# Performance work log

Measured on AMD Instinct MI355X. Metric: run time of the kernel, lower is better.

The kernel has to match this reference:

```python
import jax, jax.numpy as jnp
import numpy as np

N = 100000      # nodes
E = 1600000     # edges
F_IN = 128      # num_node_features
C = 8           # num_classes
EPS = 1e-5


def _lin_init(key, fi, fo):
    k1, k2 = jax.random.split(key)
    s = 1.0 / np.sqrt(fi)
    W = jax.random.uniform(k1, (fi, fo), jnp.float32, -s, s)
    b = jax.random.uniform(k2, (fo,), jnp.float32, -s, s)
    return W, b


def _bn_init(key, f):
    k1, k2, k3, k4 = jax.random.split(key, 4)
    gamma = 1.0 + 0.1 * jax.random.normal(k1, (f,), jnp.float32)
    beta = 0.1 * jax.random.normal(k2, (f,), jnp.float32)
    mean = 0.1 * jax.random.normal(k3, (f,), jnp.float32)
    var = jax.random.uniform(k4, (f,), jnp.float32, 0.5, 1.5)
    return gamma, beta, mean, var


def setup_inputs() -> dict:
    key = jax.random.key(0)
    ks = jax.random.split(key, 10)
    p = {}
    p["x"] = jax.random.normal(ks[0], (N, F_IN), jnp.float32)
    p["edge_index"] = jax.random.randint(ks[1], (2, E), 0, N, jnp.int32)
    p["W1"], p["b1"] = _lin_init(ks[2], F_IN, 64)
    p["g1"], p["be1"], p["m1"], p["v1"] = _bn_init(ks[3], 64)
    p["W2"], p["b2"] = _lin_init(ks[4], 64, 32)
    p["g2"], p["be2"], p["m2"], p["v2"] = _bn_init(ks[5], 32)
    p["W3"], p["b3"] = _lin_init(ks[6], 32, 16)
    p["g3"], p["be3"], p["m3"], p["v3"] = _bn_init(ks[7], 16)
    p["fcW"], p["fcb"] = _lin_init(ks[8], 16, C)
    return p


def _gcn_conv(h, W, b, src, dst, dinv):
    # GCNConv: transform, then symmetric-normalized aggregation with self-loops.
    hw = h @ W                                   # [N, Fout]
    coef = (dinv[src] * dinv[dst])[:, None]      # [E, 1]
    agg = jax.ops.segment_sum(hw[src] * coef, dst, num_segments=N)
    agg = agg + hw * (dinv * dinv)[:, None]      # self-loop contribution
    return agg + b


def _bn(h, g, be, m, v):
    # eval-mode BatchNorm1d with running stats
    return g * (h - m) * jax.lax.rsqrt(v + EPS) + be


def reference(x, edge_index, W1, b1, g1, be1, m1, v1, W2, b2, g2, be2, m2, v2,
              W3, b3, g3, be3, m3, v3, fcW, fcb):
    src, dst = edge_index[0], edge_index[1]
    deg = jax.ops.segment_sum(jnp.ones((E,), jnp.float32), dst, num_segments=N) + 1.0
    dinv = jax.lax.rsqrt(deg)                    # deg >= 1 due to self-loops

    h = jax.nn.relu(_bn(_gcn_conv(x, W1, b1, src, dst, dinv), g1, be1, m1, v1))
    h = jax.nn.relu(_bn(_gcn_conv(h, W2, b2, src, dst, dinv), g2, be2, m2, v2))
    h = jax.nn.relu(_bn(_gcn_conv(h, W3, b3, src, dst, dinv), g3, be3, m3, v3))
    return jax.nn.sigmoid(h @ fcW + fcb)
```

## Files before the change

### kernel.cpp

```cpp
#include <hip/hip_runtime.h>
#include <math.h>

static constexpr int NN = 100000;
static constexpr int NE = 1600000;
static constexpr float BN_EPS = 1e-5f;
static constexpr int K_BKT = (NN + 255) / 256;
static constexpr int CH = 4096;

typedef __attribute__((ext_vector_type(8))) short bf16x8;
typedef __attribute__((ext_vector_type(4))) float f32x4;

__device__ __forceinline__ unsigned short f2bf(float f) {
    unsigned int u = __float_as_uint(f);
    u += 0x7fffu + ((u >> 16) & 1u);
    return (unsigned short)(u >> 16);
}
__device__ __forceinline__ float bf2f(unsigned short b) {
    return __uint_as_float(((unsigned int)b) << 16);
}

__global__ __launch_bounds__(256) void bucket_hist(
    const int* __restrict__ dst, int* __restrict__ bhist, int e)
{
    __shared__ int h[K_BKT];
    for (int i = threadIdx.x; i < K_BKT; i += 256) h[i] = 0;
    __syncthreads();
    int stride = gridDim.x * 256;
    for (int i = blockIdx.x * 256 + threadIdx.x; i < e; i += stride)
        atomicAdd(&h[((unsigned)dst[i]) >> 8], 1);
    __syncthreads();
    for (int i = threadIdx.x; i < K_BKT; i += 256)
        if (h[i]) atomicAdd(&bhist[i], h[i]);
}

__global__ __launch_bounds__(256) void scan_buckets(
    const int* __restrict__ bhist, int* __restrict__ bbase, int* __restrict__ bcur)
{
    __shared__ int a[512];
    int tid = threadIdx.x;
    a[tid]       = (tid < K_BKT) ? bhist[tid] : 0;
    a[tid + 256] = (tid + 256 < K_BKT) ? bhist[tid + 256] : 0;
    __syncthreads();
    for (int d = 1; d < 512; d <<= 1) {
        int x0 = (tid >= d) ? a[tid - d] : 0;
        int i1 = tid + 256;
        int x1 = (i1 >= d) ? a[i1 - d] : 0;
        __syncthreads();
        a[tid] += x0;
        a[i1]  += x1;
        __syncthreads();
    }
    if (tid < K_BKT) {
        int ex = (tid == 0) ? 0 : a[tid - 1];
        bbase[tid] = ex; bcur[tid] = ex;
    }
    int i1 = tid + 256;
    if (i1 < K_BKT) {
        int ex = a[i1 - 1];
        bbase[i1] = ex; bcur[i1] = ex;
    }
}

__global__ __launch_bounds__(256) void partition_edges(
    const int* __restrict__ src, const int* __restrict__ dst,
    int* __restrict__ bcur, int* __restrict__ staged, int e)
{
    __shared__ int s_out[CH];
    __shared__ int cntL[512];
    __shared__ int gbase[K_BKT];
    __shared__ int curL[K_BKT];

    int tid = threadIdx.x;
    int c0 = blockIdx.x * CH;
    int cend = min(c0 + CH, e);

    for (int i = tid; i < 512; i += 256) cntL[i] = 0;
    __syncthreads();

    for (int i = c0 + tid; i < cend; i += 256)
        atomicAdd(&cntL[((unsigned)dst[i]) >> 8], 1);
    __syncthreads();

    for (int b = tid; b < K_BKT; b += 256) {
        int c = cntL[b];
        gbase[b] = (c > 0) ? atomicAdd(&bcur[b], c) : 0;
    }
    __syncthreads();

    for (int d = 1; d < 512; d <<= 1) {
        int x0 = (tid >= d) ? cntL[tid - d] : 0;
        int i1 = tid + 256;
        int x1 = (i1 >= d) ? cntL[i1 - d] : 0;
        __syncthreads();
        cntL[tid] += x0;
        cntL[i1]  += x1;
        __syncthreads();
    }
    for (int b = tid; b < K_BKT; b += 256)
        curL[b] = (b == 0) ? 0 : cntL[b - 1];
    __syncthreads();

    for (int i = c0 + tid; i < cend; i += 256) {
        int s = src[i];
        int d = dst[i];
        int b = ((unsigned)d) >> 8;
        int r = atomicAdd(&curL[b], 1);
        s_out[r] = s | ((d & 255) << 24);
    }
    __syncthreads();

    int wave = tid >> 6, lane = tid & 63;
    for (int b = wave; b < K_BKT; b += 4) {
        int lo = (b == 0) ? 0 : cntL[b - 1];
        int hi = cntL[b];
        int gb = gbase[b];
        for (int i = lo + lane; i < hi; i += 64)
            staged[gb + (i - lo)] = s_out[i];
    }
}

__global__ __launch_bounds__(256) void place_edges(
    const int* __restrict__ bbase, const int* __restrict__ staged,
    int* __restrict__ esrc, int* __restrict__ off, int* __restrict__ cnt,
    float* __restrict__ dinv, int n, int e)
{
    __shared__ int cntL[256];
    __shared__ int scn[256];
    __shared__ int curL[256];
    int b = blockIdx.x;
    int tid = threadIdx.x;
    int node0 = b << 8;
    int nN = min(256, n - node0);
    int beg = bbase[b];
    int end = (b == (int)gridDim.x - 1) ? e : bbase[b + 1];

    cntL[tid] = 0;
    __syncthreads();
    for (int i = beg + tid; i < end; i += 256)
        atomicAdd(&cntL[((unsigned)staged[i]) >> 24], 1);
    __syncthreads();
    scn[tid] = cntL[tid];
    __syncthreads();
    for (int d = 1; d < 256; d <<= 1) {
        int x = (tid >= d) ? scn[tid - d] : 0;
        __syncthreads();
        scn[tid] += x;
        __syncthreads();
    }
    int lofs = (tid == 0) ? 0 : scn[tid - 1];
    if (tid < nN) {
        int node = node0 + tid;
        off[node] = beg + lofs;
        cnt[node] = cntL[tid];
        dinv[node] = rsqrtf((float)cntL[tid] + 1.0f);
    }
    curL[tid] = beg + lofs;
    __syncthreads();
    for (int i = beg + tid; i < end; i += 256) {
        int u = staged[i];
        int pos = atomicAdd(&curL[((unsigned)u) >> 24], 1);
        esrc[pos] = u & 0x00FFFFFF;
    }
}

template<int K, int FOUT>
__device__ __forceinline__ void prep_body(
    const float* __restrict__ W, unsigned short* __restrict__ blob, int t)
{
    constexpr int CT = FOUT / 16;
    int lane = t & 63;
    int ct   = (t >> 6) % CT;
    int ks   = (t >> 6) / CT;
    int col  = ct * 16 + (lane & 15);
    int k0   = ks * 32 + (lane >> 4) * 8;

    union { bf16x8 v; unsigned short e[8]; } u;
#pragma unroll
    for (int j = 0; j < 8; ++j) {
        int kp = k0 + j;
        unsigned short r;
        if (kp < 2 * K) {
            int k = (kp < K) ? kp : kp - K;
            r = f2bf(W[k * FOUT + col]);
        } else {
            float f = W[(kp - 2 * K) * FOUT + col];
            unsigned short h = f2bf(f);
            r = f2bf(f - bf2f(h));
        }
        u.e[j] = r;
    }
    *reinterpret_cast<bf16x8*>(blob + (size_t)t * 8) = u.v;
}

__global__ __launch_bounds__(256) void prep_all(
    const float* __restrict__ W1, const float* __restrict__ W2,
    const float* __restrict__ W3, unsigned short* __restrict__ b1,
    unsigned short* __restrict__ b2, unsigned short* __restrict__ b3,
    int* __restrict__ bhist)
{
    int t = blockIdx.x * 256 + threadIdx.x;
    if (t < 3072)            prep_body<128, 64>(W1, b1, t);
    else if (t < 3840)       prep_body<64, 32>(W2, b2, t - 3072);
    else if (t < 4032)       prep_body<32, 16>(W3, b3, t - 3840);
    else if (t < 4032 + K_BKT) bhist[t - 4032] = 0;
}

template<int K, int FOUT>
__global__ __launch_bounds__(256) void gemm_mfma(
    const float* __restrict__ h, const unsigned short* __restrict__ wtb,
    const float* __restrict__ dinv, unsigned short* __restrict__ hw, int n)
{
    constexpr int PAD = 8;
    constexpr int LDA = 2 * K + PAD;
    constexpr int CT  = FOUT / 16;
    constexpr int KS  = (3 * K) / 32;
    __shared__ unsigned short As[64 * LDA];

    const int tid  = threadIdx.x;
    const int row0 = blockIdx.x * 64;

    constexpr int QK = K / 4;
    for (int i = tid; i < 64 * QK; i += 256) {
        int r = i / QK;
        int q = i % QK;
        int g = row0 + r;
        float4 v;
        if (g < n) v = *reinterpret_cast<const float4*>(h + (size_t)g * K + q * 4);
        else       v = make_float4(0.f, 0.f, 0.f, 0.f);
        ushort4 hi, lo;
        hi.x = f2bf(v.x); lo.x = f2bf(v.x - bf2f(hi.x));
        hi.y = f2bf(v.y); lo.y = f2bf(v.y - bf2f(hi.y));
        hi.z = f2bf(v.z); lo.z = f2bf(v.z - bf2f(hi.z));
        hi.w = f2bf(v.w); lo.w = f2bf(v.w - bf2f(hi.w));
        *reinterpret_cast<ushort4*>(&As[r * LDA + q * 4])     = hi;
        *reinterpret_cast<ushort4*>(&As[r * LDA + K + q * 4]) = lo;
    }
    __syncthreads();

    const int wave = tid >> 6;
    const int lane = tid & 63;
    const int l15  = lane & 15;
    const int kgrp = (lane >> 4) * 8;
    const int arow = wave * 16 + l15;

    const unsigned short* wlane = wtb + lane * 8;

    f32x4 acc[CT];
#pragma unroll
    for (int ct = 0; ct < CT; ++ct) acc[ct] = (f32x4){0.f, 0.f, 0.f, 0.f};

#pragma unroll
    for (int ks = 0; ks < KS; ++ks) {
        int kp = ks * 32 + kgrp;
        int ka = (kp >= 2 * K) ? kp - 2 * K : kp;
        bf16x8 a = *reinterpret_cast<const bf16x8*>(&As[arow * LDA + ka]);
#pragma unroll
        for (int ct = 0; ct < CT; ++ct) {
            bf16x8 b = *reinterpret_cast<const bf16x8*>(wlane + (ks * CT + ct) * 512);
            acc[ct] = __builtin_amdgcn_mfma_f32_16x16x32_bf16(a, b, acc[ct], 0, 0, 0);
        }
    }

    const int rbase = wave * 16 + (lane >> 4) * 4;
    float dv[4];
#pragma unroll
    for (int j = 0; j < 4; ++j) {
        int g = row0 + rbase + j;
        dv[j] = (g < n) ? dinv[g] : 0.f;
    }
#pragma unroll
    for (int ct = 0; ct < CT; ++ct) {
#pragma unroll
        for (int j = 0; j < 4; ++j) {
            int g = row0 + rbase + j;
            if (g < n) hw[(size_t)g * FOUT + ct * 16 + l15] = f2bf(acc[ct][j] * dv[j]);
        }
    }
}

template<int F>
__global__ __launch_bounds__(256) void gather_bn_relu(
    const int* __restrict__ off, const int* __restrict__ cnt,
    const int* __restrict__ esrc, const float* __restrict__ dinv,
    const unsigned short* __restrict__ hw, const float* __restrict__ bias,
    const float* __restrict__ g, const float* __restrict__ be,
    const float* __restrict__ m, const float* __restrict__ v,
    float* __restrict__ hout, int n)
{
    constexpr int SG  = F / 4;
    constexpr int NSG = 64 / SG;
    int node = (blockIdx.x * 256 + threadIdx.x) >> 6;
    if (node >= n) return;
    int lane = threadIdx.x & 63;
    int sg = lane / SG;
    int p  = lane % SG;

    int beg = off[node];
    int num = cnt[node];

    float sx = 0.f, sy = 0.f, sz = 0.f, sw = 0.f;
    int j = sg;
    for (; j + NSG < num; j += 2 * NSG) {
        int s0 = esrc[beg + j];
        int s1 = esrc[beg + j + NSG];
        ushort4 a = *reinterpret_cast<const ushort4*>(hw + (size_t)s0 * F + 4 * p);
        ushort4 b = *reinterpret_cast<const ushort4*>(hw + (size_t)s1 * F + 4 * p);
        sx += bf2f(a.x) + bf2f(b.x);
        sy += bf2f(a.y) + bf2f(b.y);
        sz += bf2f(a.z) + bf2f(b.z);
        sw += bf2f(a.w) + bf2f(b.w);
    }
    if (j < num) {
        int s0 = esrc[beg + j];
        ushort4 a = *reinterpret_cast<const ushort4*>(hw + (size_t)s0 * F + 4 * p);
        sx += bf2f(a.x); sy += bf2f(a.y); sz += bf2f(a.z); sw += bf2f(a.w);
    }
    if (sg == 0) {
        ushort4 a = *reinterpret_cast<const ushort4*>(hw + (size_t)node * F + 4 * p);
        sx += bf2f(a.x); sy += bf2f(a.y); sz += bf2f(a.z); sw += bf2f(a.w);
    }

#pragma unroll
    for (int d = SG; d < 64; d <<= 1) {
        sx += __shfl_xor(sx, d);
        sy += __shfl_xor(sy, d);
        sz += __shfl_xor(sz, d);
        sw += __shfl_xor(sw, d);
    }

    if (sg == 0) {
        int c0 = 4 * p;
        float4 gg = *reinterpret_cast<const float4*>(g + c0);
        float4 vv = *reinterpret_cast<const float4*>(v + c0);
        float4 bb = *reinterpret_cast<const float4*>(bias + c0);
        float4 mm = *reinterpret_cast<const float4*>(m + c0);
        float4 ee = *reinterpret_cast<const float4*>(be + c0);
        float dn = dinv[node];
        float4 y;
        y.x = fmaxf(gg.x * rsqrtf(vv.x + BN_EPS) * (dn * sx + bb.x - mm.x) + ee.x, 0.f);
        y.y = fmaxf(gg.y * rsqrtf(vv.y + BN_EPS) * (dn * sy + bb.y - mm.y) + ee.y, 0.f);
        y.z = fmaxf(gg.z * rsqrtf(vv.z + BN_EPS) * (dn * sz + bb.z - mm.z) + ee.z, 0.f);
        y.w = fmaxf(gg.w * rsqrtf(vv.w + BN_EPS) * (dn * sw + bb.w - mm.w) + ee.w, 0.f);
        *reinterpret_cast<float4*>(hout + (size_t)node * F + c0) = y;
    }
}

__global__ __launch_bounds__(256) void gather_bn_relu_fc(
    const int* __restrict__ off, const int* __restrict__ cnt,
    const int* __restrict__ esrc, const float* __restrict__ dinv,
    const unsigned short* __restrict__ hw, const float* __restrict__ bias,
    const float* __restrict__ g, const float* __restrict__ be,
    const float* __restrict__ m, const float* __restrict__ v,
    const float* __restrict__ fcW, const float* __restrict__ fcb,
    float* __restrict__ out, int n)
{
    constexpr int F = 16, SG = 4, NSG = 16;
    __shared__ float WsF[128];
    __shared__ float bsF[8];
    __shared__ float ybuf[4][16];

    int tid = threadIdx.x;
    if (tid < 128) WsF[tid] = fcW[tid];
    if (tid < 8)   bsF[tid] = fcb[tid];
    __syncthreads();

    int node = (blockIdx.x * 256 + tid) >> 6;
    int wv   = tid >> 6;
    int lane = tid & 63;
    bool act = node < n;

    if (act) {
        int sg = lane / SG;
        int p  = lane % SG;
        int beg = off[node];
        int num = cnt[node];

        float sx = 0.f, sy = 0.f, sz = 0.f, sw = 0.f;
        int j = sg;
        for (; j + NSG < num; j += 2 * NSG) {
            int s0 = esrc[beg + j];
            int s1 = esrc[beg + j + NSG];
            ushort4 a = *reinterpret_cast<const ushort4*>(hw + (size_t)s0 * F + 4 * p);
            ushort4 b = *reinterpret_cast<const ushort4*>(hw + (size_t)s1 * F + 4 * p);
            sx += bf2f(a.x) + bf2f(b.x);
            sy += bf2f(a.y) + bf2f(b.y);
            sz += bf2f(a.z) + bf2f(b.z);
            sw += bf2f(a.w) + bf2f(b.w);
        }
        if (j < num) {
            int s0 = esrc[beg + j];
            ushort4 a = *reinterpret_cast<const ushort4*>(hw + (size_t)s0 * F + 4 * p);
            sx += bf2f(a.x); sy += bf2f(a.y); sz += bf2f(a.z); sw += bf2f(a.w);
        }
        if (sg == 0) {
            ushort4 a = *reinterpret_cast<const ushort4*>(hw + (size_t)node * F + 4 * p);
            sx += bf2f(a.x); sy += bf2f(a.y); sz += bf2f(a.z); sw += bf2f(a.w);
        }

#pragma unroll
        for (int d = SG; d < 64; d <<= 1) {
            sx += __shfl_xor(sx, d);
            sy += __shfl_xor(sy, d);
            sz += __shfl_xor(sz, d);
            sw += __shfl_xor(sw, d);
        }

        if (sg == 0) {
            int c0 = 4 * p;
            float dn = dinv[node];
            float y0 = fmaxf(g[c0+0] * rsqrtf(v[c0+0] + BN_EPS) * (dn * sx + bias[c0+0] - m[c0+0]) + be[c0+0], 0.f);
            float y1 = fmaxf(g[c0+1] * rsqrtf(v[c0+1] + BN_EPS) * (dn * sy + bias[c0+1] - m[c0+1]) + be[c0+1], 0.f);
            float y2 = fmaxf(g[c0+2] * rsqrtf(v[c0+2] + BN_EPS) * (dn * sz + bias[c0+2] - m[c0+2]) + be[c0+2], 0.f);
            float y3 = fmaxf(g[c0+3] * rsqrtf(v[c0+3] + BN_EPS) * (dn * sw + bias[c0+3] - m[c0+3]) + be[c0+3], 0.f);
            ybuf[wv][c0+0] = y0;
            ybuf[wv][c0+1] = y1;
            ybuf[wv][c0+2] = y2;
            ybuf[wv][c0+3] = y3;
        }
    }
    __syncthreads();

    if (act && lane < 8) {
        float o = bsF[lane];
#pragma unroll
        for (int k = 0; k < 16; ++k) o += ybuf[wv][k] * WsF[k * 8 + lane];
        out[(size_t)node * 8 + lane] = 1.0f / (1.0f + expf(-o));
    }
}

extern "C" void kernel_launch(void* const* d_in, const int* in_sizes, int n_in,
                              void* d_out, int out_size, void* d_ws, size_t ws_size,
                              hipStream_t stream) {
    const float* x   = (const float*)d_in[0];
    const int*   ei  = (const int*)  d_in[1];
    const float* W1  = (const float*)d_in[2];
    const float* b1  = (const float*)d_in[3];
    const float* g1  = (const float*)d_in[4];
    const float* be1 = (const float*)d_in[5];
    const float* m1  = (const float*)d_in[6];
    const float* v1  = (const float*)d_in[7];
    const float* W2  = (const float*)d_in[8];
    const float* b2  = (const float*)d_in[9];
    const float* g2  = (const float*)d_in[10];
    const float* be2 = (const float*)d_in[11];
    const float* m2  = (const float*)d_in[12];
    const float* v2  = (const float*)d_in[13];
    const float* W3  = (const float*)d_in[14];
    const float* b3  = (const float*)d_in[15];
    const float* g3  = (const float*)d_in[16];
    const float* be3 = (const float*)d_in[17];
    const float* m3  = (const float*)d_in[18];
    const float* v3  = (const float*)d_in[19];
    const float* fcW = (const float*)d_in[20];
    const float* fcb = (const float*)d_in[21];
    float* out = (float*)d_out;

    const int* src = ei;
    const int* dst = ei + NE;

    char* w = (char*)d_ws;
    float* dinv  = (float*)(w + 0);
    int*   cnt   = (int*)  (w + (512 << 10));
    int*   off   = (int*)  (w + (1024 << 10));
    int*   bhist = (int*)  (w + (1536 << 10));
    int*   bbase = (int*)  (w + (1600 << 10));
    int*   bcur  = (int*)  (w + (1664 << 10));
    int*   staged= (int*)  (w + (2u << 20));
    unsigned short* wt1 = (unsigned short*)(w + (8600u << 10));
    unsigned short* wt2 = wt1 + 24576;
    unsigned short* wt3 = wt2 + 6144;
    int*   esrc  = (int*)  (w + (9u << 20));
    unsigned short* hw = (unsigned short*)(w + (16u << 20));
    float* H     = (float*)(w + (29u << 20));

    float* h1 = H;
    float* h2 = H;

    prep_all<<<(4032 + K_BKT + 255) / 256, 256, 0, stream>>>(
        W1, W2, W3, wt1, wt2, wt3, bhist);

    bucket_hist<<<256, 256, 0, stream>>>(dst, bhist, NE);
    scan_buckets<<<1, 256, 0, stream>>>(bhist, bbase, bcur);
    partition_edges<<<(NE + CH - 1) / CH, 256, 0, stream>>>(src, dst, bcur, staged, NE);
    place_edges<<<K_BKT, 256, 0, stream>>>(bbase, staged, esrc, off, cnt, dinv, NN, NE);

    const int GG = (NN * 64 + 255) / 256;

    gemm_mfma<128, 64><<<(NN + 63) / 64, 256, 0, stream>>>(x, wt1, dinv, hw, NN);
    gather_bn_relu<64><<<GG, 256, 0, stream>>>(
        off, cnt, esrc, dinv, hw, b1, g1, be1, m1, v1, h1, NN);

    gemm_mfma<64, 32><<<(NN + 63) / 64, 256, 0, stream>>>(h1, wt2, dinv, hw, NN);
    gather_bn_relu<32><<<GG, 256, 0, stream>>>(
        off, cnt, esrc, dinv, hw, b2, g2, be2, m2, v2, h2, NN);

    gemm_mfma<32, 16><<<(NN + 63) / 64, 256, 0, stream>>>(h2, wt3, dinv, hw, NN);
    gather_bn_relu_fc<<<GG, 256, 0, stream>>>(
        off, cnt, esrc, dinv, hw, b3, g3, be3, m3, v3, fcW, fcb, out, NN);
}
```

Baseline: 267.9 us.

## Fuse layer-2 and layer-3 linear transforms into preceding gather epilogues

The dense GEMMs for layers 2 and 3 are folded into the epilogues of the layer-1 and layer-2 gather kernels. Each wave stages its node's BN+ReLU output in LDS and multiplies it by the next weight matrix, which is held in shared memory. The result is written directly as a dinv-scaled bf16 row. This removes two GEMM launches, the fp32 intermediate activation round trip to global memory and the bf16 weight-split prep for W2 and W3. In exchange, each gather block now has to load the weights into LDS and does some scalar FMA work per node.

```diff
diff --git a/kernel.cpp b/kernel.cpp
--- a/kernel.cpp
+++ b/kernel.cpp
@@ -193,16 +193,12 @@
 }
 
 __global__ __launch_bounds__(256) void prep_all(
-    const float* __restrict__ W1, const float* __restrict__ W2,
-    const float* __restrict__ W3, unsigned short* __restrict__ b1,
-    unsigned short* __restrict__ b2, unsigned short* __restrict__ b3,
+    const float* __restrict__ W1, unsigned short* __restrict__ b1,
     int* __restrict__ bhist)
 {
     int t = blockIdx.x * 256 + threadIdx.x;
-    if (t < 3072)            prep_body<128, 64>(W1, b1, t);
-    else if (t < 3840)       prep_body<64, 32>(W2, b2, t - 3072);
-    else if (t < 4032)       prep_body<32, 16>(W3, b3, t - 3840);
-    else if (t < 4032 + K_BKT) bhist[t - 4032] = 0;
+    if (t < 3072)              prep_body<128, 64>(W1, b1, t);
+    else if (t < 3072 + K_BKT) bhist[t - 3072] = 0;
 }
 
 template<int K, int FOUT>
@@ -278,33 +274,40 @@
     }
 }
 
-template<int F>
-__global__ __launch_bounds__(256) void gather_bn_relu(
+__global__ __launch_bounds__(256) void gather_l1(
     const int* __restrict__ off, const int* __restrict__ cnt,
     const int* __restrict__ esrc, const float* __restrict__ dinv,
-    const unsigned short* __restrict__ hw, const float* __restrict__ bias,
+    const unsigned short* __restrict__ hw1, const float* __restrict__ bias,
     const float* __restrict__ g, const float* __restrict__ be,
     const float* __restrict__ m, const float* __restrict__ v,
-    float* __restrict__ hout, int n)
-{
-    constexpr int SG  = F / 4;
-    constexpr int NSG = 64 / SG;
-    int node = (blockIdx.x * 256 + threadIdx.x) >> 6;
+    const float* __restrict__ W2, unsigned short* __restrict__ hw2, int n)
+{
+    constexpr int F = 64, SG = 16, NSG = 4;
+    __shared__ float W2s[64 * 32];
+    __shared__ float ybuf[4][64];
+
+    int tid = threadIdx.x;
+    for (int i = tid; i < 64 * 32; i += 256) W2s[i] = W2[i];
+    __syncthreads();
+
+    int node = (blockIdx.x * 256 + tid) >> 6;
     if (node >= n) return;
-    int lane = threadIdx.x & 63;
+    int wv   = tid >> 6;
+    int lane = tid & 63;
     int sg = lane / SG;
     int p  = lane % SG;
 
     int beg = off[node];
     int num = cnt[node];
+    float dn = dinv[node];
 
     float sx = 0.f, sy = 0.f, sz = 0.f, sw = 0.f;
     int j = sg;
     for (; j + NSG < num; j += 2 * NSG) {
         int s0 = esrc[beg + j];
         int s1 = esrc[beg + j + NSG];
-        ushort4 a = *reinterpret_cast<const ushort4*>(hw + (size_t)s0 * F + 4 * p);
-        ushort4 b = *reinterpret_cast<const ushort4*>(hw + (size_t)s1 * F + 4 * p);
+        ushort4 a = *reinterpret_cast<const ushort4*>(hw1 + (size_t)s0 * F + 4 * p);
+        ushort4 b = *reinterpret_cast<const ushort4*>(hw1 + (size_t)s1 * F + 4 * p);
         sx += bf2f(a.x) + bf2f(b.x);
         sy += bf2f(a.y) + bf2f(b.y);
         sz += bf2f(a.z) + bf2f(b.z);
@@ -312,11 +315,11 @@
     }
     if (j < num) {
         int s0 = esrc[beg + j];
-        ushort4 a = *reinterpret_cast<const ushort4*>(hw + (size_t)s0 * F + 4 * p);
+        ushort4 a = *reinterpret_cast<const ushort4*>(hw1 + (size_t)s0 * F + 4 * p);
         sx += bf2f(a.x); sy += bf2f(a.y); sz += bf2f(a.z); sw += bf2f(a.w);
     }
     if (sg == 0) {
-        ushort4 a = *reinterpret_cast<const ushort4*>(hw + (size_t)node * F + 4 * p);
+        ushort4 a = *reinterpret_cast<const ushort4*>(hw1 + (size_t)node * F + 4 * p);
         sx += bf2f(a.x); sy += bf2f(a.y); sz += bf2f(a.z); sw += bf2f(a.w);
     }
 
@@ -335,14 +338,101 @@
         float4 bb = *reinterpret_cast<const float4*>(bias + c0);
         float4 mm = *reinterpret_cast<const float4*>(m + c0);
         float4 ee = *reinterpret_cast<const float4*>(be + c0);
-        float dn = dinv[node];
-        float4 y;
-        y.x = fmaxf(gg.x * rsqrtf(vv.x + BN_EPS) * (dn * sx + bb.x - mm.x) + ee.x, 0.f);
-        y.y = fmaxf(gg.y * rsqrtf(vv.y + BN_EPS) * (dn * sy + bb.y - mm.y) + ee.y, 0.f);
-        y.z = fmaxf(gg.z * rsqrtf(vv.z + BN_EPS) * (dn * sz + bb.z - mm.z) + ee.z, 0.f);
-        y.w = fmaxf(gg.w * rsqrtf(vv.w + BN_EPS) * (dn * sw + bb.w - mm.w) + ee.w, 0.f);
-        *reinterpret_cast<float4*>(hout + (size_t)node * F + c0) = y;
-    }
+        ybuf[wv][c0+0] = fmaxf(gg.x * rsqrtf(vv.x + BN_EPS) * (dn * sx + bb.x - mm.x) + ee.x, 0.f);
+        ybuf[wv][c0+1] = fmaxf(gg.y * rsqrtf(vv.y + BN_EPS) * (dn * sy + bb.y - mm.y) + ee.y, 0.f);
+        ybuf[wv][c0+2] = fmaxf(gg.z * rsqrtf(vv.z + BN_EPS) * (dn * sz + bb.z - mm.z) + ee.z, 0.f);
+        ybuf[wv][c0+3] = fmaxf(gg.w * rsqrtf(vv.w + BN_EPS) * (dn * sw + bb.w - mm.w) + ee.w, 0.f);
+    }
+
+    int c  = lane & 31;
+    int kh = (lane >> 5) * 32;
+    float acc = 0.f;
+#pragma unroll
+    for (int k = 0; k < 32; ++k)
+        acc += ybuf[wv][kh + k] * W2s[(kh + k) * 32 + c];
+    acc += __shfl_xor(acc, 32);
+    if (lane < 32) hw2[(size_t)node * 32 + c] = f2bf(acc * dn);
+}
+
+__global__ __launch_bounds__(256) void gather_l2(
+    const int* __restrict__ off, const int* __restrict__ cnt,
+    const int* __restrict__ esrc, const float* __restrict__ dinv,
+    const unsigned short* __restrict__ hw2, const float* __restrict__ bias,
+    const float* __restrict__ g, const float* __restrict__ be,
+    const float* __restrict__ m, const float* __restrict__ v,
+    const float* __restrict__ W3, unsigned short* __restrict__ hw3, int n)
+{
+    constexpr int F = 32, SG = 8, NSG = 8;
+    __shared__ float W3s[32 * 16];
+    __shared__ float ybuf[4][32];
+
+    int tid = threadIdx.x;
+    for (int i = tid; i < 32 * 16; i += 256) W3s[i] = W3[i];
+    __syncthreads();
+
+    int node = (blockIdx.x * 256 + tid) >> 6;
+    if (node >= n) return;
+    int wv   = tid >> 6;
+    int lane = tid & 63;
+    int sg = lane / SG;
+    int p  = lane % SG;
+
+    int beg = off[node];
+    int num = cnt[node];
+    float dn = dinv[node];
+
+    float sx = 0.f, sy = 0.f, sz = 0.f, sw = 0.f;
+    int j = sg;
+    for (; j + NSG < num; j += 2 * NSG) {
+        int s0 = esrc[beg + j];
+        int s1 = esrc[beg + j + NSG];
+        ushort4 a = *reinterpret_cast<const ushort4*>(hw2 + (size_t)s0 * F + 4 * p);
+        ushort4 b = *reinterpret_cast<const ushort4*>(hw2 + (size_t)s1 * F + 4 * p);
+        sx += bf2f(a.x) + bf2f(b.x);
+        sy += bf2f(a.y) + bf2f(b.y);
+        sz += bf2f(a.z) + bf2f(b.z);
+        sw += bf2f(a.w) + bf2f(b.w);
+    }
+    if (j < num) {
+        int s0 = esrc[beg + j];
+        ushort4 a = *reinterpret_cast<const ushort4*>(hw2 + (size_t)s0 * F + 4 * p);
+        sx += bf2f(a.x); sy += bf2f(a.y); sz += bf2f(a.z); sw += bf2f(a.w);
+    }
+    if (sg == 0) {
+        ushort4 a = *reinterpret_cast<const ushort4*>(hw2 + (size_t)node * F + 4 * p);
+        sx += bf2f(a.x); sy += bf2f(a.y); sz += bf2f(a.z); sw += bf2f(a.w);
+    }
+
+#pragma unroll
+    for (int d = SG; d < 64; d <<= 1) {
+        sx += __shfl_xor(sx, d);
+        sy += __shfl_xor(sy, d);
+        sz += __shfl_xor(sz, d);
+        sw += __shfl_xor(sw, d);
+    }
+
+    if (sg == 0) {
+        int c0 = 4 * p;
+        float4 gg = *reinterpret_cast<const float4*>(g + c0);
+        float4 vv = *reinterpret_cast<const float4*>(v + c0);
+        float4 bb = *reinterpret_cast<const float4*>(bias + c0);
+        float4 mm = *reinterpret_cast<const float4*>(m + c0);
+        float4 ee = *reinterpret_cast<const float4*>(be + c0);
+        ybuf[wv][c0+0] = fmaxf(gg.x * rsqrtf(vv.x + BN_EPS) * (dn * sx + bb.x - mm.x) + ee.x, 0.f);
+        ybuf[wv][c0+1] = fmaxf(gg.y * rsqrtf(vv.y + BN_EPS) * (dn * sy + bb.y - mm.y) + ee.y, 0.f);
+        ybuf[wv][c0+2] = fmaxf(gg.z * rsqrtf(vv.z + BN_EPS) * (dn * sz + bb.z - mm.z) + ee.z, 0.f);
+        ybuf[wv][c0+3] = fmaxf(gg.w * rsqrtf(vv.w + BN_EPS) * (dn * sw + bb.w - mm.w) + ee.w, 0.f);
+    }
+
+    int c  = lane & 15;
+    int kq = (lane >> 4) * 8;
+    float acc = 0.f;
+#pragma unroll
+    for (int k = 0; k < 8; ++k)
+        acc += ybuf[wv][kq + k] * W3s[(kq + k) * 16 + c];
+    acc += __shfl_xor(acc, 16);
+    acc += __shfl_xor(acc, 32);
+    if (lane < 16) hw3[(size_t)node * 16 + c] = f2bf(acc * dn);
 }
 
 __global__ __launch_bounds__(256) void gather_bn_relu_fc(
@@ -408,14 +498,10 @@
         if (sg == 0) {
             int c0 = 4 * p;
             float dn = dinv[node];
-            float y0 = fmaxf(g[c0+0] * rsqrtf(v[c0+0] + BN_EPS) * (dn * sx + bias[c0+0] - m[c0+0]) + be[c0+0], 0.f);
-            float y1 = fmaxf(g[c0+1] * rsqrtf(v[c0+1] + BN_EPS) * (dn * sy + bias[c0+1] - m[c0+1]) + be[c0+1], 0.f);
-            float y2 = fmaxf(g[c0+2] * rsqrtf(v[c0+2] + BN_EPS) * (dn * sz + bias[c0+2] - m[c0+2]) + be[c0+2], 0.f);
-            float y3 = fmaxf(g[c0+3] * rsqrtf(v[c0+3] + BN_EPS) * (dn * sw + bias[c0+3] - m[c0+3]) + be[c0+3], 0.f);
-            ybuf[wv][c0+0] = y0;
-            ybuf[wv][c0+1] = y1;
-            ybuf[wv][c0+2] = y2;
-            ybuf[wv][c0+3] = y3;
+            ybuf[wv][c0+0] = fmaxf(g[c0+0] * rsqrtf(v[c0+0] + BN_EPS) * (dn * sx + bias[c0+0] - m[c0+0]) + be[c0+0], 0.f);
+            ybuf[wv][c0+1] = fmaxf(g[c0+1] * rsqrtf(v[c0+1] + BN_EPS) * (dn * sy + bias[c0+1] - m[c0+1]) + be[c0+1], 0.f);
+            ybuf[wv][c0+2] = fmaxf(g[c0+2] * rsqrtf(v[c0+2] + BN_EPS) * (dn * sz + bias[c0+2] - m[c0+2]) + be[c0+2], 0.f);
+            ybuf[wv][c0+3] = fmaxf(g[c0+3] * rsqrtf(v[c0+3] + BN_EPS) * (dn * sw + bias[c0+3] - m[c0+3]) + be[c0+3], 0.f);
         }
     }
     __syncthreads();
@@ -467,17 +553,12 @@
     int*   bcur  = (int*)  (w + (1664 << 10));
     int*   staged= (int*)  (w + (2u << 20));
     unsigned short* wt1 = (unsigned short*)(w + (8600u << 10));
-    unsigned short* wt2 = wt1 + 24576;
-    unsigned short* wt3 = wt2 + 6144;
     int*   esrc  = (int*)  (w + (9u << 20));
-    unsigned short* hw = (unsigned short*)(w + (16u << 20));
-    float* H     = (float*)(w + (29u << 20));
-
-    float* h1 = H;
-    float* h2 = H;
-
-    prep_all<<<(4032 + K_BKT + 255) / 256, 256, 0, stream>>>(
-        W1, W2, W3, wt1, wt2, wt3, bhist);
+    unsigned short* hw1 = (unsigned short*)(w + (16u << 20));
+    unsigned short* hw2 = (unsigned short*)(w + (30u << 20));
+    unsigned short* hw3 = (unsigned short*)(w + (38u << 20));
+
+    prep_all<<<(3072 + K_BKT + 255) / 256, 256, 0, stream>>>(W1, wt1, bhist);
 
     bucket_hist<<<256, 256, 0, stream>>>(dst, bhist, NE);
     scan_buckets<<<1, 256, 0, stream>>>(bhist, bbase, bcur);
@@ -486,15 +567,13 @@
 
     const int GG = (NN * 64 + 255) / 256;
 
-    gemm_mfma<128, 64><<<(NN + 63) / 64, 256, 0, stream>>>(x, wt1, dinv, hw, NN);
-    gather_bn_relu<64><<<GG, 256, 0, stream>>>(
-        off, cnt, esrc, dinv, hw, b1, g1, be1, m1, v1, h1, NN);
-
-    gemm_mfma<64, 32><<<(NN + 63) / 64, 256, 0, stream>>>(h1, wt2, dinv, hw, NN);
-    gather_bn_relu<32><<<GG, 256, 0, stream>>>(
-        off, cnt, esrc, dinv, hw, b2, g2, be2, m2, v2, h2, NN);
-
-    gemm_mfma<32, 16><<<(NN + 63) / 64, 256, 0, stream>>>(h2, wt3, dinv, hw, NN);
+    gemm_mfma<128, 64><<<(NN + 63) / 64, 256, 0, stream>>>(x, wt1, dinv, hw1, NN);
+    gather_l1<<<GG, 256, 0, stream>>>(
+        off, cnt, esrc, dinv, hw1, b1, g1, be1, m1, v1, W2, hw2, NN);
+
+    gather_l2<<<GG, 256, 0, stream>>>(
+        off, cnt, esrc, dinv, hw2, b2, g2, be2, m2, v2, W3, hw3, NN);
+
     gather_bn_relu_fc<<<GG, 256, 0, stream>>>(
-        off, cnt, esrc, dinv, hw, b3, g3, be3, m3, v3, fcW, fcb, out, NN);
-}
+        off, cnt, esrc, dinv, hw3, b3, g3, be3, m3, v3, fcW, fcb, out, NN);
+}
```

Measured after the change: 275.9 us. +3.0%, slower.
